# Kernel tuning notes

Measured on AMD Instinct MI355X. Metric: run time of the kernel, lower is better.

The kernel has to match this reference:

```python
import jax, jax.numpy as jnp
import numpy as np
from functools import partial

TAU = 2.0
V_TH = 1.0
ALPHA = 2.0  # ATan surrogate alpha (spikingjelly default)
DIM = 512

@jax.custom_vjp
def heaviside(x):
    return (x >= 0).astype(x.dtype)

def _heaviside_fwd(x):
    return heaviside(x), x

def _heaviside_bwd(x, g):
    # ATan surrogate: d/dx sigmoid-like = alpha/2 / (1 + (pi/2*alpha*x)^2)
    sg = (ALPHA / 2.0) / (1.0 + (jnp.pi / 2.0 * ALPHA * x) ** 2)
    return (g * sg,)

heaviside.defvjp(_heaviside_fwd, _heaviside_bwd)

def lif_multistep(x_seq):
    """LIF, decay_input=False, hard reset to 0, v_threshold=V_TH.
    x_seq: [T, ...] -> spikes [T, ...]"""
    decay = 1.0 - 1.0 / TAU
    def step(v, x):
        v = v * decay + x            # charge (no decay on input)
        s = heaviside(v - V_TH)      # fire with surrogate grad
        v = v * (1.0 - jax.lax.stop_gradient(s))  # hard reset, detach_reset
        return v, s
    v0 = jnp.zeros_like(x_seq[0])
    _, s_seq = jax.lax.scan(step, v0, x_seq)
    return s_seq

def setup_inputs() -> dict:
    key = jax.random.key(0)
    k1, k2, k3 = jax.random.split(key, 3)
    T, B, N = 4, 32, 512
    inputs = jax.random.normal(k1, (T, B, N, 2 * DIM), dtype=jnp.float32)
    W = jax.random.normal(k2, (DIM, DIM), dtype=jnp.float32) / np.sqrt(DIM)
    b = jax.random.normal(k3, (DIM,), dtype=jnp.float32) * 0.01
    return {"inputs": inputs, "W": W, "b": b}

def reference(inputs, W, b):
    outputs, gate = jnp.split(inputs, 2, axis=-1)   # chunk(2, dim=-1)
    gate = lif_multistep(gate)                      # lif1
    gate = jnp.einsum('tbnd,ed->tbne', gate, W) + b # proj_conv (Linear)
    gate = lif_multistep(gate)                      # lif2
    return outputs * gate
```

## Files before the change

kernel.cpp:

```cpp
#include <hip/hip_runtime.h>
#include <cstdint>
#include <cstddef>

#define TS     4
#define BNROWS 16384
#define DIMN   512
#define CIN    1024

typedef __attribute__((ext_vector_type(8))) short short8;
typedef __attribute__((ext_vector_type(4))) float f32x4;

__device__ __forceinline__ uint16_t f2bf(float f) {
    union { float f; uint32_t u; } x; x.f = f;
    return (uint16_t)((x.u + 0x7FFFu + ((x.u >> 16) & 1u)) >> 16);
}
__device__ __forceinline__ float bf2f(uint16_t h) {
    union { uint32_t u; float f; } x; x.u = ((uint32_t)h) << 16;
    return x.f;
}

__global__ __launch_bounds__(256) void k_wsplit(const float* __restrict__ W,
        uint16_t* __restrict__ Wh, uint16_t* __restrict__ Wm) {
    int i = (blockIdx.x * 256 + threadIdx.x) * 4;
    int e  = i >> 9;
    int k  = i & 511;
    int ks = k >> 5, kk = k & 31;
    size_t o = ((size_t)((ks << 9) + e) << 5) + kk;
    float4 w4 = *(const float4*)(W + i);
    float wv[4] = {w4.x, w4.y, w4.z, w4.w};
    uint16_t hh[4], mm[4];
#pragma unroll
    for (int j = 0; j < 4; ++j) {
        uint16_t a = f2bf(wv[j]);
        float r = wv[j] - bf2f(a);
        hh[j] = a; mm[j] = f2bf(r);
    }
    *(ushort4*)(Wh + o) = make_ushort4(hh[0], hh[1], hh[2], hh[3]);
    *(ushort4*)(Wm + o) = make_ushort4(mm[0], mm[1], mm[2], mm[3]);
}

#define DELTA 1e-3f
__global__ __launch_bounds__(512, 4) void k_fused(
        const float*    __restrict__ in,
        const uint16_t* __restrict__ Wh,
        const uint16_t* __restrict__ Wm,
        const float*    __restrict__ bias,
        float*          __restrict__ out,
        uint8_t*        __restrict__ A8,
        unsigned int*   __restrict__ counter,
        unsigned int*   __restrict__ list,
        unsigned int    cap) {
    __shared__ short A_lds[64 * 512];
    __shared__ unsigned short gate_bits[64 * 32];

    const int tid = threadIdx.x;
    const int blk = blockIdx.x;
    const int bn0 = blk * 16;

#pragma unroll
    for (int pp = 0; pp < 2; ++pp) {
        const int p   = tid + pp * 512;
        const int bnl = p >> 6;
        const int g   = p & 63;
        const int d0  = g << 3;
        const int bng = bn0 + bnl;
        float v[8] = {0.f,0.f,0.f,0.f,0.f,0.f,0.f,0.f};
#pragma unroll
        for (int t = 0; t < TS; ++t) {
            const float4* px = (const float4*)(in + ((size_t)(t * BNROWS + bng)) * CIN + DIMN + d0);
            float4 x0 = px[0], x1 = px[1];
            float xs[8] = {x0.x, x0.y, x0.z, x0.w, x1.x, x1.y, x1.z, x1.w};
            short8 sb;
            union { uint2 u; uint8_t b[8]; } pk;
#pragma unroll
            for (int j = 0; j < 8; ++j) {
                v[j] = v[j] * 0.5f + xs[j];
                bool sp = (v[j] >= 1.0f);
                sb[j]   = sp ? (short)0x3F80 : (short)0;
                pk.b[j] = sp ? 1u : 0u;
                v[j] = sp ? 0.0f : v[j];
            }
            const int row  = (bnl << 2) + t;
            const int boff = row * 1024 + ((d0 * 2) ^ ((row & 7) << 4));
            *(short8*)((char*)A_lds + boff) = sb;
            *(uint2*)(A8 + ((size_t)((bng << 2) + t)) * DIMN + d0) = pk.u;
        }
    }
    __syncthreads();

    const int wv   = tid >> 6;
    const int lane = tid & 63;
    const int ln   = lane & 15;
    const int quad = lane >> 4;
    const int e_base = wv * 64;

    f32x4 acc[4][4] = {};

#pragma unroll 4
    for (int ks = 0; ks < 16; ++ks) {
        short8 bh[4], bm[4];
#pragma unroll
        for (int ni = 0; ni < 4; ++ni) {
            const size_t off = ((size_t)((ks << 9) + e_base + ni * 16 + ln) << 5) + quad * 8;
            bh[ni] = *(const short8*)(Wh + off);
            bm[ni] = *(const short8*)(Wm + off);
        }
        const int k0 = ks * 32 + quad * 8;
        short8 a[4];
#pragma unroll
        for (int mi = 0; mi < 4; ++mi) {
            const int row  = mi * 16 + ln;
            const int boff = row * 1024 + ((k0 * 2) ^ ((row & 7) << 4));
            a[mi] = *(const short8*)((const char*)A_lds + boff);
        }
#pragma unroll
        for (int ni = 0; ni < 4; ++ni) {
#pragma unroll
            for (int mi = 0; mi < 4; ++mi) {
                acc[mi][ni] = __builtin_amdgcn_mfma_f32_16x16x32_bf16(a[mi], bh[ni], acc[mi][ni], 0, 0, 0);
                acc[mi][ni] = __builtin_amdgcn_mfma_f32_16x16x32_bf16(a[mi], bm[ni], acc[mi][ni], 0, 0, 0);
            }
        }
    }

#pragma unroll
    for (int ni = 0; ni < 4; ++ni) {
        const int e = e_base + ni * 16 + ln;
        const float be = bias[e];
#pragma unroll
        for (int mi = 0; mi < 4; ++mi) {
            const int bn = bn0 + mi * 4 + quad;
            float v = 0.f;
            bool bad = false;
#pragma unroll
            for (int t = 0; t < TS; ++t) {
                float y = acc[mi][ni][t] + be;
                v = v * 0.5f + y;
                bad = bad || (fabsf(v - 1.0f) < DELTA);
                bool sp = (v >= 1.0f);
                unsigned long long b = __ballot(sp);
                if (ln == 0) {
                    const int row_l = (mi * 4 + quad) * 4 + t;
                    gate_bits[row_l * 32 + (wv * 4 + ni)] =
                        (unsigned short)((b >> (quad * 16)) & 0xFFFFull);
                }
                v = sp ? 0.0f : v;
            }
            if (bad) {
                unsigned idx = atomicAdd(counter, 1u);
                if (idx < cap) list[idx] = ((unsigned)bn << 9) | (unsigned)e;
            }
        }
    }
    __syncthreads();

#pragma unroll
    for (int it = 0; it < 16; ++it) {
        const int s   = it * 512 + tid;
        const int t   = s >> 11;
        const int bnl = (s >> 7) & 15;
        const int c   = s & 127;
        const size_t rbase = (size_t)(t * BNROWS + bn0 + bnl);
        const float4 ov = *(const float4*)(in + rbase * CIN + (c << 2));
        const unsigned gb = gate_bits[(bnl * 4 + t) * 32 + (c >> 2)];
        const int sh = (c & 3) * 4;
        float4 o;
        o.x = ((gb >> (sh + 0)) & 1u) ? ov.x : 0.0f;
        o.y = ((gb >> (sh + 1)) & 1u) ? ov.y : 0.0f;
        o.z = ((gb >> (sh + 2)) & 1u) ? ov.z : 0.0f;
        o.w = ((gb >> (sh + 3)) & 1u) ? ov.w : 0.0f;
        *(float4*)(out + rbase * DIMN + (c << 2)) = o;
    }
}

__global__ __launch_bounds__(256) void k_fix(
        const uint8_t* __restrict__ A8,
        const float*   __restrict__ W,
        const float*   __restrict__ bias,
        const float*   __restrict__ in,
        float*         __restrict__ out,
        const unsigned int* __restrict__ counter,
        const unsigned int* __restrict__ list,
        unsigned int cap) {
    unsigned n = *counter; if (n > cap) n = cap;
    unsigned gtid = blockIdx.x * blockDim.x + threadIdx.x;
    unsigned gsz  = gridDim.x * blockDim.x;
    for (unsigned i = gtid; i < n; i += gsz) {
        unsigned item = list[i];
        int bn = (int)(item >> 9), e = (int)(item & 511u);
        const float* wrow = W + (size_t)e * DIMN;
        float v = 0.f;
        for (int t = 0; t < TS; ++t) {
            const uint8_t* arow = A8 + (size_t)(bn * 4 + t) * DIMN;
            float acc0 = 0.f, acc1 = 0.f, acc2 = 0.f, acc3 = 0.f;
            for (int c = 0; c < 32; ++c) {
                const int base = c * 16;
#pragma unroll
                for (int j = 3; j >= 0; --j) {
                    const int b4 = base + j * 4;
                    float s0 = arow[b4 + 0] ? 1.0f : 0.0f;
                    float s1 = arow[b4 + 1] ? 1.0f : 0.0f;
                    float s2 = arow[b4 + 2] ? 1.0f : 0.0f;
                    float s3 = arow[b4 + 3] ? 1.0f : 0.0f;
                    acc0 = fmaf(s0, wrow[b4 + 0], acc0);
                    acc1 = fmaf(s1, wrow[b4 + 1], acc1);
                    acc2 = fmaf(s2, wrow[b4 + 2], acc2);
                    acc3 = fmaf(s3, wrow[b4 + 3], acc3);
                }
            }
            float lo  = acc0 + acc1;
            float hi  = acc2 + acc3;
            float dot = lo + hi;
            float y = dot + bias[e];
            v = v * 0.5f + y;
            bool sp = (v >= 1.0f);
            size_t obase = (size_t)(t * BNROWS + bn);
            out[obase * DIMN + e] = sp ? in[obase * CIN + e] : 0.0f;
            v = sp ? 0.0f : v;
        }
    }
}

extern "C" void kernel_launch(void* const* d_in, const int* in_sizes, int n_in,
                              void* d_out, int out_size, void* d_ws, size_t ws_size,
                              hipStream_t stream) {
    const float* in   = (const float*)d_in[0];
    const float* W    = (const float*)d_in[1];
    const float* bias = (const float*)d_in[2];
    float* out = (float*)d_out;

    uint8_t*  A8 = (uint8_t*)d_ws;
    uint16_t* Wh = (uint16_t*)((char*)d_ws + (size_t)33554432);
    uint16_t* Wm = (uint16_t*)((char*)d_ws + (size_t)34078720);
    unsigned int* counter = (unsigned int*)((char*)d_ws + (size_t)34603008);
    unsigned int* list    = (unsigned int*)((char*)d_ws + (size_t)34603072);
    const unsigned int cap = 1000000u;

    hipMemsetAsync(counter, 0, sizeof(unsigned int), stream);
    k_wsplit<<<256, 256, 0, stream>>>(W, Wh, Wm);
    k_fused<<<1024, 512, 0, stream>>>(in, Wh, Wm, bias, out, A8, counter, list, cap);
    k_fix<<<256, 256, 0, stream>>>(A8, W, bias, in, out, counter, list, cap);
}
```

Measured before the change: 606.3 us.

## Split gate-multiply epilogue out of fused kernel into separate streaming kernel

After: 609.4 us. About the same (+0.5%).

```diff
diff --git a/kernel.cpp b/kernel.cpp
--- a/kernel.cpp
+++ b/kernel.cpp
@@ -45,13 +45,12 @@
         const uint16_t* __restrict__ Wh,
         const uint16_t* __restrict__ Wm,
         const float*    __restrict__ bias,
-        float*          __restrict__ out,
+        unsigned short* __restrict__ gbits,
         uint8_t*        __restrict__ A8,
         unsigned int*   __restrict__ counter,
         unsigned int*   __restrict__ list,
         unsigned int    cap) {
     __shared__ short A_lds[64 * 512];
-    __shared__ unsigned short gate_bits[64 * 32];
 
     const int tid = threadIdx.x;
     const int blk = blockIdx.x;
@@ -140,8 +139,7 @@
                 bool sp = (v >= 1.0f);
                 unsigned long long b = __ballot(sp);
                 if (ln == 0) {
-                    const int row_l = (mi * 4 + quad) * 4 + t;
-                    gate_bits[row_l * 32 + (wv * 4 + ni)] =
+                    gbits[((size_t)(bn * 4 + t)) * 32 + (wv * 4 + ni)] =
                         (unsigned short)((b >> (quad * 16)) & 0xFFFFull);
                 }
                 v = sp ? 0.0f : v;
@@ -152,24 +150,29 @@
             }
         }
     }
-    __syncthreads();
-
-#pragma unroll
-    for (int it = 0; it < 16; ++it) {
-        const int s   = it * 512 + tid;
-        const int t   = s >> 11;
-        const int bnl = (s >> 7) & 15;
-        const int c   = s & 127;
-        const size_t rbase = (size_t)(t * BNROWS + bn0 + bnl);
-        const float4 ov = *(const float4*)(in + rbase * CIN + (c << 2));
-        const unsigned gb = gate_bits[(bnl * 4 + t) * 32 + (c >> 2)];
-        const int sh = (c & 3) * 4;
+}
+
+__global__ __launch_bounds__(256) void k_gate(
+        const float*          __restrict__ in,
+        const unsigned short* __restrict__ gbits,
+        float*                __restrict__ out) {
+    const unsigned gtid = blockIdx.x * 256 + threadIdx.x;
+    const int bn = (gtid >> 7) & 16383;
+    const int c  = gtid & 127;
+    const unsigned gidx = ((unsigned)bn * 4) * 32 + (c >> 2);
+    const int sh = (c & 3) * 4;
+    const float4* __restrict__ in4  = (const float4*)in;
+    float4*       __restrict__ out4 = (float4*)out;
+#pragma unroll
+    for (int t = 0; t < TS; ++t) {
+        const float4 ov = in4[(size_t)(t * BNROWS + bn) * 256 + c];
+        const unsigned gb = gbits[gidx + t * 32] >> sh;
         float4 o;
-        o.x = ((gb >> (sh + 0)) & 1u) ? ov.x : 0.0f;
-        o.y = ((gb >> (sh + 1)) & 1u) ? ov.y : 0.0f;
-        o.z = ((gb >> (sh + 2)) & 1u) ? ov.z : 0.0f;
-        o.w = ((gb >> (sh + 3)) & 1u) ? ov.w : 0.0f;
-        *(float4*)(out + rbase * DIMN + (c << 2)) = o;
+        o.x = (gb & 1u) ? ov.x : 0.0f;
+        o.y = (gb & 2u) ? ov.y : 0.0f;
+        o.z = (gb & 4u) ? ov.z : 0.0f;
+        o.w = (gb & 8u) ? ov.w : 0.0f;
+        out4[(size_t)t * 2097152 + gtid] = o;
     }
 }
 
@@ -229,15 +232,17 @@
     const float* bias = (const float*)d_in[2];
     float* out = (float*)d_out;
 
-    uint8_t*  A8 = (uint8_t*)d_ws;
-    uint16_t* Wh = (uint16_t*)((char*)d_ws + (size_t)33554432);
-    uint16_t* Wm = (uint16_t*)((char*)d_ws + (size_t)34078720);
-    unsigned int* counter = (unsigned int*)((char*)d_ws + (size_t)34603008);
-    unsigned int* list    = (unsigned int*)((char*)d_ws + (size_t)34603072);
-    const unsigned int cap = 1000000u;
+    uint8_t*        A8      = (uint8_t*)d_ws;
+    uint16_t*       Wh      = (uint16_t*)((char*)d_ws + (size_t)33554432);
+    uint16_t*       Wm      = (uint16_t*)((char*)d_ws + (size_t)34078720);
+    unsigned int*   counter = (unsigned int*)((char*)d_ws + (size_t)34603008);
+    unsigned int*   list    = (unsigned int*)((char*)d_ws + (size_t)34603072);
+    unsigned short* gbits   = (unsigned short*)((char*)d_ws + (size_t)35403072);
+    const unsigned int cap = 200000u;
 
     hipMemsetAsync(counter, 0, sizeof(unsigned int), stream);
     k_wsplit<<<256, 256, 0, stream>>>(W, Wh, Wm);
-    k_fused<<<1024, 512, 0, stream>>>(in, Wh, Wm, bias, out, A8, counter, list, cap);
+    k_fused<<<1024, 512, 0, stream>>>(in, Wh, Wm, bias, gbits, A8, counter, list, cap);
+    k_gate<<<8192, 256, 0, stream>>>(in, gbits, out);
     k_fix<<<256, 256, 0, stream>>>(A8, W, bias, in, out, counter, list, cap);
 }
```
